# Optimization experiments

Hardware: AMD Instinct MI355X
Metric: run time of the kernel (lower is better)

Reference implementation:

```python
import jax, jax.numpy as jnp
import numpy as np

B, C, H, W = 32, 3, 224, 224
P = 14            # n_patches per side
PS = H // P       # 16
D = 768           # embed_size
NH = 12           # heads
DH = D // NH      # 64
L = 12            # n_blocks
FF = 4 * D
OUT = 1000
S = P * P + 1     # 197 tokens


def positional_encoding(seq_len, d):
    i = jnp.arange(seq_len, dtype=jnp.float32)[:, None]
    j = jnp.arange(d, dtype=jnp.float32)[None, :]
    je = jnp.where(j % 2 == 0, j, j - 1)
    ang = i / jnp.power(10000.0, je / d)
    return jnp.where(j % 2 == 0, jnp.sin(ang), jnp.cos(ang))


def layernorm(x, g, b, eps=1e-5):
    mu = jnp.mean(x, axis=-1, keepdims=True)
    var = jnp.var(x, axis=-1, keepdims=True)
    return (x - mu) * jax.lax.rsqrt(var + eps) * g + b


def setup_inputs() -> dict:
    key = jax.random.key(0)
    ks = jax.random.split(key, 20)
    s = 0.02
    inp = {
        'images': jax.random.normal(ks[0], (B, C, H, W), jnp.float32),
        'W_patch': jax.random.normal(ks[1], (D, C * PS * PS), jnp.float32) * s,
        'b_patch': jnp.zeros((D,), jnp.float32),
        'class_token': jax.random.uniform(ks[2], (1, D), jnp.float32),
        'ln1_g': jnp.ones((L, D), jnp.float32),
        'ln1_b': jnp.zeros((L, D), jnp.float32),
        'Wq': jax.random.normal(ks[3], (L, NH, DH, DH), jnp.float32) * s,
        'bq': jnp.zeros((L, NH, DH), jnp.float32),
        'Wk': jax.random.normal(ks[4], (L, NH, DH, DH), jnp.float32) * s,
        'bk': jnp.zeros((L, NH, DH), jnp.float32),
        'Wv': jax.random.normal(ks[5], (L, NH, DH, DH), jnp.float32) * s,
        'bv': jnp.zeros((L, NH, DH), jnp.float32),
        'ln2_g': jnp.ones((L, D), jnp.float32),
        'ln2_b': jnp.zeros((L, D), jnp.float32),
        'W1': jax.random.normal(ks[6], (L, FF, D), jnp.float32) * s,
        'b1': jnp.zeros((L, FF), jnp.float32),
        'W2': jax.random.normal(ks[7], (L, D, FF), jnp.float32) * s,
        'b2': jnp.zeros((L, D), jnp.float32),
        'Wo': jax.random.normal(ks[8], (OUT, D), jnp.float32) * s,
        'bo': jnp.zeros((OUT,), jnp.float32),
    }
    return inp


def reference(images, W_patch, b_patch, class_token, ln1_g, ln1_b,
              Wq, bq, Wk, bk, Wv, bv, ln2_g, ln2_b, W1, b1, W2, b2, Wo, bo):
    b = images.shape[0]
    # patch extraction: [B,C,P,ps,P,ps] -> [B,P*P, C*ps*ps] (flatten order C,h,w)
    patches = images.reshape(b, C, P, PS, P, PS).transpose(0, 2, 4, 1, 3, 5)
    patches = patches.reshape(b, P * P, C * PS * PS)
    tokens = patches @ W_patch.T + b_patch                     # [B, P^2, D]
    cls = jnp.broadcast_to(class_token[None], (b, 1, D))
    x = jnp.concatenate([cls, tokens], axis=1)                 # [B, S, D]
    x = x + positional_encoding(S, D)

    scale = 1.0 / jnp.sqrt(jnp.float32(DH))
    for l in range(L):
        h = layernorm(x, ln1_g[l], ln1_b[l])
        hh = h.reshape(b, S, NH, DH)
        q = jnp.einsum('bshd,hed->bshe', hh, Wq[l]) + bq[l]
        k = jnp.einsum('bshd,hed->bshe', hh, Wk[l]) + bk[l]
        v = jnp.einsum('bshd,hed->bshe', hh, Wv[l]) + bv[l]
        scores = jnp.einsum('bshe,bthe->bhst', q, k) * scale   # [B,H,S,S]
        attn = jax.nn.softmax(scores, axis=-1)
        o = jnp.einsum('bhst,bthe->bshe', attn, v).reshape(b, S, D)
        x = x + o
        h2 = layernorm(x, ln2_g[l], ln2_b[l])
        ff = jax.nn.gelu(h2 @ W1[l].T + b1[l], approximate=False) @ W2[l].T + b2[l]
        x = x + ff

    logits = x[:, 0] @ Wo.T + bo                               # [B, OUT]
    return jax.nn.softmax(logits, axis=-1)
```

## Files before the change

### kernel.cpp

```cpp
#include <hip/hip_runtime.h>
#include <math.h>

static constexpr int kB   = 32;
static constexpr int kC   = 3;
static constexpr int kH   = 224;
static constexpr int kW   = 224;
static constexpr int kP   = 14;
static constexpr int kPS  = 16;
static constexpr int kD   = 768;
static constexpr int kNH  = 12;
static constexpr int kDH  = 64;
static constexpr int kL   = 12;
static constexpr int kFF  = 3072;
static constexpr int kOUT = 1000;
static constexpr int kS   = 197;
static constexpr int kTOK = kB * kS;
static constexpr int kNP  = kP * kP;
static constexpr int kMP  = 6400;
static constexpr int kQKV = 3 * kD;

typedef unsigned short u16;
typedef __attribute__((ext_vector_type(4))) float f32x4;
typedef __attribute__((ext_vector_type(8))) short bf16x8;

__device__ __forceinline__ u16 f2bf(float x) {
    unsigned u = __float_as_uint(x);
    return (u16)((u + 0x7FFFu + ((u >> 16) & 1u)) >> 16);
}
__device__ __forceinline__ float bf2f(u16 x) {
    return __uint_as_float((unsigned)x << 16);
}
__device__ __forceinline__ void cp16_async(void* lds, const void* g) {
    __builtin_amdgcn_global_load_lds((const __attribute__((address_space(1))) unsigned*)g,
                                     (__attribute__((address_space(3))) unsigned*)lds,
                                     16, 0, 0);
}
__device__ __forceinline__ float gelu_f(float v) {
    float z = v * 0.70710678118654752f;
    float s = fabsf(z);
    float t = 1.0f / (1.0f + 0.3275911f * s);
    float p = t * (0.254829592f + t * (-0.284496736f +
              t * (1.421413741f + t * (-1.453152027f + t * 1.061405429f))));
    float e = p * __expf(-s * s);
    float erfv = (z < 0.0f) ? (e - 1.0f) : (1.0f - e);
    return 0.5f * v * (1.0f + erfv);
}

__global__ void vit_posenc(float* __restrict__ pos) {
    int idx = blockIdx.x * 256 + threadIdx.x;
    if (idx >= kS * kD) return;
    int s = idx / kD, d = idx % kD;
    int je = d & ~1;
    double p = pow(10000.0, (double)je / (double)kD);
    float ang = (float)((double)s / p);
    pos[idx] = (d & 1) ? cosf(ang) : sinf(ang);
}

__global__ void vit_im2col_bf16(const float* __restrict__ img, u16* __restrict__ patches) {
    long idx = (long)blockIdx.x * 256 + threadIdx.x;
    if (idx >= (long)kMP * kD) return;
    int col = (int)(idx % kD);
    long rp = idx / kD;
    if (rp >= (long)kB * kNP) { patches[idx] = 0; return; }
    int p = (int)(rp % kNP), b = (int)(rp / kNP);
    int c = col >> 8;
    int rem = col & 255;
    int i = rem >> 4, j = rem & 15;
    int py = p / kP, px = p % kP;
    patches[idx] = f2bf(img[(((long)b * kC + c) * kH + py * kPS + i) * kW + px * kPS + j]);
}

__global__ void vit_assemble(const float* __restrict__ tokens, const float* __restrict__ cls,
                             const float* __restrict__ pos, float* __restrict__ x) {
    long idx = (long)blockIdx.x * 256 + threadIdx.x;
    if (idx >= (long)kMP * kD) return;
    int d = (int)(idx % kD);
    long bs = idx / kD;
    if (bs >= kTOK) { x[idx] = 0.0f; return; }
    int s = (int)(bs % kS);
    long b = bs / kS;
    float v = (s == 0) ? cls[d] : tokens[((long)b * kNP + (s - 1)) * kD + d];
    x[idx] = v + pos[s * kD + d];
}

__global__ void cast_bf16(const float* __restrict__ in, u16* __restrict__ out, long n4) {
    long i = (long)blockIdx.x * 256 + threadIdx.x;
    if (i >= n4) return;
    float4 v = *(const float4*)(in + i * 4);
    *(ushort4*)(out + i * 4) = make_ushort4(f2bf(v.x), f2bf(v.y), f2bf(v.z), f2bf(v.w));
}
__global__ void cast2_bf16(const float* __restrict__ in1, const float* __restrict__ in2,
                           u16* __restrict__ out1, u16* __restrict__ out2, long n4each) {
    long i = (long)blockIdx.x * 256 + threadIdx.x;
    if (i >= 2 * n4each) return;
    const float* in = (i < n4each) ? in1 : in2;
    u16* out        = (i < n4each) ? out1 : out2;
    long j          = (i < n4each) ? i : i - n4each;
    float4 v = *(const float4*)(in + j * 4);
    *(ushort4*)(out + j * 4) = make_ushort4(f2bf(v.x), f2bf(v.y), f2bf(v.z), f2bf(v.w));
}

__global__ void zero_u16(u16* __restrict__ p, long n) {
    long i = (long)blockIdx.x * 256 + threadIdx.x;
    if (i < n) p[i] = 0;
}

__global__ void build_whb_all(const float* __restrict__ Wq, const float* __restrict__ Wk,
                              const float* __restrict__ Wv, const float* __restrict__ bq,
                              const float* __restrict__ bk, const float* __restrict__ bv,
                              u16* __restrict__ Wh, float* __restrict__ bh) {
    int idx = blockIdx.x * 256 + threadIdx.x;
    if (idx >= kL * kNH * 192 * 64) return;
    int d  = idx & 63;
    int r  = (idx >> 6) % 192;
    int lh = (idx >> 6) / 192;
    int sec = r >> 6, e = r & 63;
    const float* W = (sec == 0) ? Wq : (sec == 1) ? Wk : Wv;
    Wh[idx] = f2bf(W[((long)lh * 64 + e) * 64 + d]);
    if (d == 0) {
        const float* bs = (sec == 0) ? bq : (sec == 1) ? bk : bv;
        bh[lh * 192 + r] = bs[lh * 64 + e];
    }
}

__global__ __launch_bounds__(256) void vit_ln(const float* __restrict__ x,
                                              const float* __restrict__ g,
                                              const float* __restrict__ b,
                                              u16* __restrict__ out) {
    long t = blockIdx.x;
    const float* xr = x + t * kD;
    int tid = threadIdx.x;
    float v0 = xr[tid], v1 = xr[tid + 256], v2 = xr[tid + 512];
    float s  = v0 + v1 + v2;
    float sq = v0 * v0 + v1 * v1 + v2 * v2;
    #pragma unroll
    for (int o = 32; o; o >>= 1) { s += __shfl_xor(s, o); sq += __shfl_xor(sq, o); }
    __shared__ float red[8];
    int wid = tid >> 6, lane = tid & 63;
    if (lane == 0) { red[wid] = s; red[4 + wid] = sq; }
    __syncthreads();
    s  = red[0] + red[1] + red[2] + red[3];
    sq = red[4] + red[5] + red[6] + red[7];
    float mu  = s * (1.0f / kD);
    float var = sq * (1.0f / kD) - mu * mu;
    float rs  = rsqrtf(var + 1e-5f);
    u16* orow = out + t * kD;
    orow[tid]       = f2bf((v0 - mu) * rs * g[tid]       + b[tid]);
    orow[tid + 256] = f2bf((v1 - mu) * rs * g[tid + 256] + b[tid + 256]);
    orow[tid + 512] = f2bf((v2 - mu) * rs * g[tid + 512] + b[tid + 512]);
}

template <int EPI>
__global__ __launch_bounds__(256) void mm_bt(const u16* __restrict__ A, int lda,
                                             const u16* __restrict__ B, int ldb,
                                             const float* __restrict__ bias,
                                             const float* X, void* Cout, int ldc, int K) {
    __shared__ __align__(16) u16 As[3][4096];
    __shared__ __align__(16) u16 Bs[3][4096];

    const int gx = gridDim.x, gy = gridDim.y;
    const int nwg = gx * gy;
    const int disp = blockIdx.y * gx + blockIdx.x;
    const int q8 = nwg >> 3, r8 = nwg & 7;
    const int xcd = disp & 7, lot = disp >> 3;
    const int work = (xcd < r8 ? xcd * (q8 + 1) : r8 * (q8 + 1) + (xcd - r8) * q8) + lot;
    const int row0 = (work / gy) << 7;
    const int col0 = (work % gy) << 7;

    const int tid  = threadIdx.x;
    const int lane = tid & 63;
    const int wm = ((tid >> 6) >> 1) << 6;
    const int wn = ((tid >> 6) & 1) << 6;
    const int lr = lane & 15, lhi = lane >> 4;

    const int srow = tid >> 2;
    const int sch  = (((tid & 3) ^ ((srow >> 1) & 3)) << 3);
    const u16* Ag = A + (long)(row0 + srow) * lda + sch;
    const u16* Bg = B + (long)(col0 + srow) * ldb + sch;
    const long Astep = 64L * lda, Bstep = 64L * ldb;
    const int ldst = tid << 3;

    auto stage = [&](int buf, int k0) {
        cp16_async(&As[buf][ldst],        Ag + k0);
        cp16_async(&As[buf][ldst + 2048], Ag + Astep + k0);
        cp16_async(&Bs[buf][ldst],        Bg + k0);
        cp16_async(&Bs[buf][ldst + 2048], Bg + Bstep + k0);
    };
    stage(0, 0);
    stage(1, 32);

    f32x4 acc[4][4] = {};
    const int nk = K >> 5;
    const int rch = (lhi ^ ((lr >> 1) & 3)) << 3;
    int cur = 0;
    for (int t = 0; t < nk; t++) {
        if (t + 1 < nk) asm volatile("s_waitcnt vmcnt(4)" ::: "memory");
        else            asm volatile("s_waitcnt vmcnt(0)" ::: "memory");
        __builtin_amdgcn_sched_barrier(0);
        __builtin_amdgcn_s_barrier();
        bf16x8 af[4], bfr[4];
        #pragma unroll
        for (int m = 0; m < 4; m++)
            af[m] = *(const bf16x8*)&As[cur][(wm + (m << 4) + lr) * 32 + rch];
        #pragma unroll
        for (int n = 0; n < 4; n++)
            bfr[n] = *(const bf16x8*)&Bs[cur][(wn + (n << 4) + lr) * 32 + rch];
        if (t + 2 < nk) {
            int nb = cur + 2; if (nb >= 3) nb -= 3;
            stage(nb, (t + 2) << 5);
        }
        #pragma unroll
        for (int m = 0; m < 4; m++)
            #pragma unroll
            for (int n = 0; n < 4; n++)
                acc[m][n] = __builtin_amdgcn_mfma_f32_16x16x32_bf16(af[m], bfr[n], acc[m][n], 0, 0, 0);
        __builtin_amdgcn_s_barrier();
        cur = (cur + 1 == 3) ? 0 : cur + 1;
    }

    const int r0 = wm + (lhi << 2);
    const int cb = wn + lr;
    #pragma unroll
    for (int n = 0; n < 4; n++) {
        const int cc = col0 + cb + (n << 4);
        const float bv = bias[cc];
        #pragma unroll
        for (int m = 0; m < 4; m++) {
            #pragma unroll
            for (int r = 0; r < 4; r++) {
                const long idx = (long)(row0 + r0 + (m << 4) + r) * ldc + cc;
                float v = acc[m][n][r] + bv;
                if (EPI == 1) {
                    ((u16*)Cout)[idx] = f2bf(gelu_f(v));
                } else if (EPI == 2) {
                    ((float*)Cout)[idx] = v + X[idx];
                } else if (EPI == 3) {
                    ((u16*)Cout)[idx] = f2bf(v);
                } else {
                    ((float*)Cout)[idx] = v;
                }
            }
        }
    }
}

__global__ __launch_bounds__(256) void mm_qkv(const u16* __restrict__ hbm,
                                              const u16* __restrict__ Wh,
                                              const float* __restrict__ bh,
                                              u16* __restrict__ qkv) {
    const int h = blockIdx.y;
    const int row0 = blockIdx.x << 6;
    const int tid = threadIdx.x, lane = tid & 63, wave = tid >> 6;
    const int l15 = lane & 15, lhi = lane >> 4;
    const u16* Ab = hbm + h * kDH + (lhi << 3);
    const u16* Bb = Wh + (long)h * 192 * 64 + (lhi << 3);

    bf16x8 af[4][2];
    #pragma unroll
    for (int m = 0; m < 4; m++) {
        const u16* ap = Ab + (long)(row0 + (m << 4) + l15) * kD;
        af[m][0] = *(const bf16x8*)ap;
        af[m][1] = *(const bf16x8*)(ap + 32);
    }
    bf16x8 bfr[3][2];
    #pragma unroll
    for (int n = 0; n < 3; n++) {
        const u16* bp = Bb + (long)(wave * 48 + (n << 4) + l15) * 64;
        bfr[n][0] = *(const bf16x8*)bp;
        bfr[n][1] = *(const bf16x8*)(bp + 32);
    }
    f32x4 acc[4][3] = {};
    __builtin_amdgcn_s_setprio(1);
    #pragma unroll
    for (int m = 0; m < 4; m++)
        #pragma unroll
        for (int n = 0; n < 3; n++) {
            acc[m][n] = __builtin_amdgcn_mfma_f32_16x16x32_bf16(af[m][0], bfr[n][0], acc[m][n], 0, 0, 0);
            acc[m][n] = __builtin_amdgcn_mfma_f32_16x16x32_bf16(af[m][1], bfr[n][1], acc[m][n], 0, 0, 0);
        }
    __builtin_amdgcn_s_setprio(0);
    #pragma unroll
    for (int n = 0; n < 3; n++) {
        const int c = wave * 48 + (n << 4) + l15;
        const int sec = c >> 6, e = c & 63;
        const float bv = bh[h * 192 + c];
        const long gcol = (long)sec * kD + h * kDH + e;
        #pragma unroll
        for (int m = 0; m < 4; m++)
            #pragma unroll
            for (int i = 0; i < 4; i++) {
                const int r = row0 + (m << 4) + (lhi << 2) + i;
                qkv[(long)r * kQKV + gcol] = f2bf(acc[m][n][i] + bv);
            }
    }
}

__global__ __launch_bounds__(256) void vit_attn_fused(const u16* __restrict__ qkv,
                                                      float* __restrict__ x) {
    constexpr int SP = 224;
    constexpr int NT = 13;
    constexpr int LDP = 232;
    __shared__ u16 Plds[64][LDP];
    __shared__ u16 Vt[64][LDP];

    const int z = blockIdx.y, qt = blockIdx.x;
    const int b = z / kNH, h = z % kNH;
    const u16* base = qkv + (long)b * kS * kQKV;
    const u16* Qg = base + h * kDH;
    const u16* Kg = base + kD + h * kDH;
    const u16* Vg = base + 2 * kD + h * kDH;
    const int tid = threadIdx.x, lane = tid & 63, wave = tid >> 6;
    const int l15 = lane & 15, lhi = lane >> 4;

    for (int i = tid; i < (SP * kDH) / 4; i += 256) {
        int s  = i >> 4;
        int d0 = (i & 15) << 2;
        ushort4 v = *(const ushort4*)(Vg + (long)s * kQKV + d0);
        Vt[d0 + 0][s] = v.x; Vt[d0 + 1][s] = v.y;
        Vt[d0 + 2][s] = v.z; Vt[d0 + 3][s] = v.w;
    }

    const int qrow = (qt << 6) + (wave << 4) + l15;
    const u16* qrp = Qg + (long)qrow * kQKV + (lhi << 3);
    const bf16x8 qf0 = *(const bf16x8*)(qrp);
    const bf16x8 qf1 = *(const bf16x8*)(qrp + 32);

    f32x4 sc[NT];
    const u16* krp = Kg + (long)l15 * kQKV + (lhi << 3);
    __builtin_amdgcn_s_setprio(1);
    #pragma unroll
    for (int t = 0; t < NT; t++) {
        const u16* kp = krp + (long)(t << 4) * kQKV;
        bf16x8 kb0 = *(const bf16x8*)(kp);
        bf16x8 kb1 = *(const bf16x8*)(kp + 32);
        f32x4 a = {0.0f, 0.0f, 0.0f, 0.0f};
        a = __builtin_amdgcn_mfma_f32_16x16x32_bf16(qf0, kb0, a, 0, 0, 0);
        a = __builtin_amdgcn_mfma_f32_16x16x32_bf16(qf1, kb1, a, 0, 0, 0);
        sc[t] = a;
    }
    __builtin_amdgcn_s_setprio(0);

    float mx[4] = {-1e30f, -1e30f, -1e30f, -1e30f};
    #pragma unroll
    for (int t = 0; t < NT; t++) {
        const int c = (t << 4) + l15;
        #pragma unroll
        for (int q = 0; q < 4; q++) {
            float v = (c < kS) ? sc[t][q] * 0.125f : -1e30f;
            sc[t][q] = v;
            mx[q] = fmaxf(mx[q], v);
        }
    }
    #pragma unroll
    for (int o = 1; o < 16; o <<= 1)
        #pragma unroll
        for (int q = 0; q < 4; q++) mx[q] = fmaxf(mx[q], __shfl_xor(mx[q], o));
    float sum[4] = {0.0f, 0.0f, 0.0f, 0.0f};
    #pragma unroll
    for (int t = 0; t < NT; t++)
        #pragma unroll
        for (int q = 0; q < 4; q++) {
            float e = __expf(sc[t][q] - mx[q]);
            sc[t][q] = e;
            sum[q] += e;
        }
    #pragma unroll
    for (int o = 1; o < 16; o <<= 1)
        #pragma unroll
        for (int q = 0; q < 4; q++) sum[q] += __shfl_xor(sum[q], o);

    const int prow = (wave << 4) + (lhi << 2);
    #pragma unroll
    for (int t = 0; t < NT; t++)
        #pragma unroll
        for (int q = 0; q < 4; q++)
            Plds[prow + q][(t << 4) + l15] = f2bf(sc[t][q]);
    #pragma unroll
    for (int q = 0; q < 4; q++)
        Plds[prow + q][208 + l15] = 0;
    __syncthreads();

    f32x4 oacc[4] = {};
    const int arow = (wave << 4) + l15;
    const int koff = lhi << 3;
    __builtin_amdgcn_s_setprio(1);
    #pragma unroll
    for (int ks = 0; ks < 7; ks++) {
        bf16x8 pa = *(const bf16x8*)&Plds[arow][ks * 32 + koff];
        #pragma unroll
        for (int n = 0; n < 4; n++) {
            bf16x8 vb = *(const bf16x8*)&Vt[(n << 4) + l15][ks * 32 + koff];
            oacc[n] = __builtin_amdgcn_mfma_f32_16x16x32_bf16(pa, vb, oacc[n], 0, 0, 0);
        }
    }
    __builtin_amdgcn_s_setprio(0);

    const int orow0 = (qt << 6) + (wave << 4) + (lhi << 2);
    #pragma unroll
    for (int q = 0; q < 4; q++) {
        const int r = orow0 + q;
        if (r >= kS) continue;
        const float rinv = 1.0f / sum[q];
        float* xp = x + ((long)b * kS + r) * kD + h * kDH + l15;
        #pragma unroll
        for (int n = 0; n < 4; n++)
            xp[n << 4] += oacc[n][q] * rinv;
    }
}

template <int ACT, int RES>
__global__ __launch_bounds__(256) void vit_gemm(const float* __restrict__ A, long lda, long sAz,
                                                const float* __restrict__ B, long ldb, long sBz,
                                                const float* __restrict__ bias, long sbz,
                                                const float* __restrict__ R,
                                                float* __restrict__ C, long ldc, long sCz,
                                                int M, int N, int K) {
    __shared__ __align__(16) float As[16][64];
    __shared__ __align__(16) float Bs[16][64];
    long z = blockIdx.z;
    A += z * sAz;  B += z * sBz;  C += z * sCz;
    if (bias) bias += z * sbz;
    const float* Rp = nullptr;
    if (RES) Rp = R + z * sCz;

    int row0 = blockIdx.x * 64, col0 = blockIdx.y * 64;
    int tid = threadIdx.x;
    int lr = tid >> 2, lk = (tid & 3) << 2;
    int tm = tid >> 4, tn = tid & 15;
    float acc[4][4] = {};

    for (int k0 = 0; k0 < K; k0 += 16) {
        float4 a = {0, 0, 0, 0}, bb = {0, 0, 0, 0};
        int gr = row0 + lr;
        if (gr < M) a = *(const float4*)(A + (long)gr * lda + k0 + lk);
        int gc = col0 + lr;
        if (gc < N) bb = *(const float4*)(B + (long)gc * ldb + k0 + lk);
        __syncthreads();
        As[lk + 0][lr] = a.x;  As[lk + 1][lr] = a.y;  As[lk + 2][lr] = a.z;  As[lk + 3][lr] = a.w;
        Bs[lk + 0][lr] = bb.x; Bs[lk + 1][lr] = bb.y; Bs[lk + 2][lr] = bb.z; Bs[lk + 3][lr] = bb.w;
        __syncthreads();
        #pragma unroll
        for (int k = 0; k < 16; k++) {
            const float4 av = *reinterpret_cast<const float4*>(&As[k][tm << 2]);
            const float4 bv = *reinterpret_cast<const float4*>(&Bs[k][tn << 2]);
            float aa[4] = {av.x, av.y, av.z, av.w};
            float bw[4] = {bv.x, bv.y, bv.z, bv.w};
            #pragma unroll
            for (int i = 0; i < 4; i++)
                #pragma unroll
                for (int j = 0; j < 4; j++)
                    acc[i][j] = fmaf(aa[i], bw[j], acc[i][j]);
        }
    }
    #pragma unroll
    for (int i = 0; i < 4; i++) {
        int r = row0 + (tm << 2) + i;
        if (r >= M) continue;
        #pragma unroll
        for (int j = 0; j < 4; j++) {
            int c = col0 + (tn << 2) + j;
            if (c >= N) continue;
            float v = acc[i][j];
            if (bias) v += bias[c];
            if (ACT == 1) v = gelu_f(v);
            if (RES) v += Rp[(long)r * ldc + c];
            C[(long)r * ldc + c] = v;
        }
    }
}

__global__ __launch_bounds__(256) void vit_smout(const float* __restrict__ logits,
                                                 float* __restrict__ out) {
    int b = blockIdx.x;
    const float* p = logits + (long)b * kOUT;
    int tid = threadIdx.x;
    float v[4];
    float mx = -1e30f;
    #pragma unroll
    for (int i = 0; i < 4; i++) {
        int c = tid + (i << 8);
        v[i] = (c < kOUT) ? p[c] : -1e30f;
        mx = fmaxf(mx, v[i]);
    }
    #pragma unroll
    for (int o = 32; o; o >>= 1) mx = fmaxf(mx, __shfl_xor(mx, o));
    __shared__ float red[8];
    int wid = tid >> 6, lane = tid & 63;
    if (lane == 0) red[wid] = mx;
    __syncthreads();
    mx = fmaxf(fmaxf(red[0], red[1]), fmaxf(red[2], red[3]));
    float sum = 0.0f;
    #pragma unroll
    for (int i = 0; i < 4; i++) {
        int c = tid + (i << 8);
        if (c < kOUT) { v[i] = expf(v[i] - mx); sum += v[i]; }
    }
    #pragma unroll
    for (int o = 32; o; o >>= 1) sum += __shfl_xor(sum, o);
    __syncthreads();
    if (lane == 0) red[4 + wid] = sum;
    __syncthreads();
    sum = red[4] + red[5] + red[6] + red[7];
    float inv = 1.0f / sum;
    #pragma unroll
    for (int i = 0; i < 4; i++) {
        int c = tid + (i << 8);
        if (c < kOUT) out[(long)b * kOUT + c] = v[i] * inv;
    }
}

extern "C" void kernel_launch(void* const* d_in, const int* in_sizes, int n_in,
                              void* d_out, int out_size, void* d_ws, size_t ws_size,
                              hipStream_t stream) {
    (void)in_sizes; (void)n_in; (void)out_size;
    const float* images  = (const float*)d_in[0];
    const float* W_patch = (const float*)d_in[1];
    const float* b_patch = (const float*)d_in[2];
    const float* cls     = (const float*)d_in[3];
    const float* ln1_g   = (const float*)d_in[4];
    const float* ln1_b   = (const float*)d_in[5];
    const float* Wq      = (const float*)d_in[6];
    const float* bq      = (const float*)d_in[7];
    const float* Wk      = (const float*)d_in[8];
    const float* bk      = (const float*)d_in[9];
    const float* Wv      = (const float*)d_in[10];
    const float* bv      = (const float*)d_in[11];
    const float* ln2_g   = (const float*)d_in[12];
    const float* ln2_b   = (const float*)d_in[13];
    const float* W1      = (const float*)d_in[14];
    const float* b1      = (const float*)d_in[15];
    const float* W2      = (const float*)d_in[16];
    const float* b2      = (const float*)d_in[17];
    const float* Wo      = (const float*)d_in[18];
    const float* bo      = (const float*)d_in[19];

    char* wsB = (char*)d_ws;
    auto alloc = [&](size_t bytes) { char* p = wsB; wsB += (bytes + 255) & ~(size_t)255; return p; };
    float* pos    = (float*)alloc((size_t)kS * kD * 4);
    float* x      = (float*)alloc((size_t)kMP * kD * 4);
    u16*   hb     = (u16*)  alloc((size_t)kMP * kD * 2);
    u16*   qkvb   = (u16*)  alloc((size_t)kMP * kQKV * 2);
    u16*   ff1b   = (u16*)  alloc((size_t)kMP * kFF * 2);
    u16*   Whb    = (u16*)  alloc((size_t)kL * kNH * 192 * 64 * 2);
    u16*   Wpb    = (u16*)  alloc((size_t)kD * kD * 2);
    float* bhb    = (float*)alloc((size_t)kL * kNH * 192 * 4);
    float* logits = (float*)alloc((size_t)kB * kOUT * 4);

    const size_t perW  = (size_t)kFF * kD;
    const size_t used  = (size_t)(wsB - (char*)d_ws);
    const bool   hoist = ws_size >= used + 2 * kL * perW * 2 + (1u << 20);
    u16* W12b = (u16*)alloc(hoist ? 2 * kL * perW * 2 : 2 * perW * 2);

    float* tokens   = (float*)qkvb;
    u16*   patchesb = ff1b;

    vit_posenc<<<(kS * kD + 255) / 256, 256, 0, stream>>>(pos);
    vit_im2col_bf16<<<(int)(((long)kMP * kD) / 256), 256, 0, stream>>>(images, patchesb);
    cast_bf16<<<(kD * kD / 4 + 255) / 256, 256, 0, stream>>>(W_patch, Wpb, (long)kD * kD / 4);
    build_whb_all<<<(kL * kNH * 192 * 64 + 255) / 256, 256, 0, stream>>>(
        Wq, Wk, Wv, bq, bk, bv, Whb, bhb);
    zero_u16<<<(96 * kD + 255) / 256, 256, 0, stream>>>(hb + (long)kTOK * kD, 96L * kD);
    if (hoist)
        cast2_bf16<<<(int)((2 * kL * perW / 4 + 255) / 256), 256, 0, stream>>>(
            W1, W2, W12b, W12b + kL * perW, (long)kL * perW / 4);
    mm_bt<0><<<dim3(kMP / 128, kD / 128), 256, 0, stream>>>(
        patchesb, kD, Wpb, kD, b_patch, nullptr, tokens, kD, kD);
    vit_assemble<<<(int)(((long)kMP * kD) / 256), 256, 0, stream>>>(tokens, cls, pos, x);

    for (int l = 0; l < kL; l++) {
        u16* W1l = hoist ? (W12b + (size_t)l * perW)            : W12b;
        u16* W2l = hoist ? (W12b + (size_t)(kL + l) * perW)     : W12b + perW;
        if (!hoist)
            cast2_bf16<<<(int)((2 * perW / 4 + 255) / 256), 256, 0, stream>>>(
                W1 + (size_t)l * perW, W2 + (size_t)l * perW, W1l, W2l, (long)perW / 4);

        vit_ln<<<kTOK, 256, 0, stream>>>(x, ln1_g + (long)l * kD, ln1_b + (long)l * kD, hb);
        mm_qkv<<<dim3(kMP / 64, kNH), 256, 0, stream>>>(
            hb, Whb + (long)l * kNH * 192 * 64, bhb + (long)l * kNH * 192, qkvb);

        vit_attn_fused<<<dim3(4, kB * kNH), 256, 0, stream>>>(qkvb, x);

        vit_ln<<<kTOK, 256, 0, stream>>>(x, ln2_g + (long)l * kD, ln2_b + (long)l * kD, hb);
        mm_bt<1><<<dim3(kMP / 128, kFF / 128), 256, 0, stream>>>(
            hb, kD, W1l, kD, b1 + (long)l * kFF, nullptr, ff1b, kFF, kD);
        mm_bt<2><<<dim3(kMP / 128, kD / 128), 256, 0, stream>>>(
            ff1b, kFF, W2l, kFF, b2 + (long)l * kD, x, x, kD, kFF);
    }

    vit_gemm<0, 0><<<dim3(1, 16, 1), 256, 0, stream>>>(
        x, (long)kS * kD, 0, Wo, kD, 0, bo, 0, nullptr,
        logits, kOUT, 0, kB, kOUT, kD);
    vit_smout<<<kB, 256, 0, stream>>>(logits, (float*)d_out);
}
```

Measured before the change: 2.533 ms.

## Add 128x256 tile GEMM with XCD-aware scheduling for FF1

Adds mm_bt2, a 512-thread GEMM with a 128x256 output tile and three-stage async LDS staging. It remaps workgroups so consecutive tiles land on the same XCD, and the FF1 projection now uses it. The larger tile is meant to improve operand reuse and L2 locality, at the cost of more LDS per block and fewer blocks per CU. It also makes the weight cast a grid-stride loop with a fixed 2048 blocks and computes positional encoding in float with __expf instead of double pow, which may shift precision slightly.

```diff
diff --git a/kernel.cpp b/kernel.cpp
--- a/kernel.cpp
+++ b/kernel.cpp
@@ -51,8 +51,7 @@
     if (idx >= kS * kD) return;
     int s = idx / kD, d = idx % kD;
     int je = d & ~1;
-    double p = pow(10000.0, (double)je / (double)kD);
-    float ang = (float)((double)s / p);
+    float ang = (float)s * __expf((float)je * (-9.210340371976184f / 768.0f));
     pos[idx] = (d & 1) ? cosf(ang) : sinf(ang);
 }
 
@@ -91,13 +90,14 @@
 }
 __global__ void cast2_bf16(const float* __restrict__ in1, const float* __restrict__ in2,
                            u16* __restrict__ out1, u16* __restrict__ out2, long n4each) {
-    long i = (long)blockIdx.x * 256 + threadIdx.x;
-    if (i >= 2 * n4each) return;
-    const float* in = (i < n4each) ? in1 : in2;
-    u16* out        = (i < n4each) ? out1 : out2;
-    long j          = (i < n4each) ? i : i - n4each;
-    float4 v = *(const float4*)(in + j * 4);
-    *(ushort4*)(out + j * 4) = make_ushort4(f2bf(v.x), f2bf(v.y), f2bf(v.z), f2bf(v.w));
+    const long stride = (long)gridDim.x * 256;
+    for (long i = (long)blockIdx.x * 256 + threadIdx.x; i < 2 * n4each; i += stride) {
+        const float* in = (i < n4each) ? in1 : in2;
+        u16* out        = (i < n4each) ? out1 : out2;
+        long j          = (i < n4each) ? i : i - n4each;
+        float4 v = *(const float4*)(in + j * 4);
+        *(ushort4*)(out + j * 4) = make_ushort4(f2bf(v.x), f2bf(v.y), f2bf(v.z), f2bf(v.w));
+    }
 }
 
 __global__ void zero_u16(u16* __restrict__ p, long n) {
@@ -195,6 +195,100 @@
     int cur = 0;
     for (int t = 0; t < nk; t++) {
         if (t + 1 < nk) asm volatile("s_waitcnt vmcnt(4)" ::: "memory");
+        else            asm volatile("s_waitcnt vmcnt(0)" ::: "memory");
+        __builtin_amdgcn_sched_barrier(0);
+        __builtin_amdgcn_s_barrier();
+        bf16x8 af[4], bfr[4];
+        #pragma unroll
+        for (int m = 0; m < 4; m++)
+            af[m] = *(const bf16x8*)&As[cur][(wm + (m << 4) + lr) * 32 + rch];
+        #pragma unroll
+        for (int n = 0; n < 4; n++)
+            bfr[n] = *(const bf16x8*)&Bs[cur][(wn + (n << 4) + lr) * 32 + rch];
+        if (t + 2 < nk) {
+            int nb = cur + 2; if (nb >= 3) nb -= 3;
+            stage(nb, (t + 2) << 5);
+        }
+        #pragma unroll
+        for (int m = 0; m < 4; m++)
+            #pragma unroll
+            for (int n = 0; n < 4; n++)
+                acc[m][n] = __builtin_amdgcn_mfma_f32_16x16x32_bf16(af[m], bfr[n], acc[m][n], 0, 0, 0);
+        __builtin_amdgcn_s_barrier();
+        cur = (cur + 1 == 3) ? 0 : cur + 1;
+    }
+
+    const int r0 = wm + (lhi << 2);
+    const int cb = wn + lr;
+    #pragma unroll
+    for (int n = 0; n < 4; n++) {
+        const int cc = col0 + cb + (n << 4);
+        const float bv = bias[cc];
+        #pragma unroll
+        for (int m = 0; m < 4; m++) {
+            #pragma unroll
+            for (int r = 0; r < 4; r++) {
+                const long idx = (long)(row0 + r0 + (m << 4) + r) * ldc + cc;
+                float v = acc[m][n][r] + bv;
+                if (EPI == 1) {
+                    ((u16*)Cout)[idx] = f2bf(gelu_f(v));
+                } else if (EPI == 2) {
+                    ((float*)Cout)[idx] = v + X[idx];
+                } else if (EPI == 3) {
+                    ((u16*)Cout)[idx] = f2bf(v);
+                } else {
+                    ((float*)Cout)[idx] = v;
+                }
+            }
+        }
+    }
+}
+
+template <int EPI>
+__global__ __launch_bounds__(512, 4) void mm_bt2(const u16* __restrict__ A, int lda,
+                                                 const u16* __restrict__ B, int ldb,
+                                                 const float* __restrict__ bias,
+                                                 const float* X, void* Cout, int ldc, int K) {
+    __shared__ __align__(16) u16 As[3][4096];
+    __shared__ __align__(16) u16 Bs[3][8192];
+
+    const int gx = gridDim.x, gy = gridDim.y;
+    const int nwg = gx * gy;
+    const int disp = blockIdx.y * gx + blockIdx.x;
+    const int q8 = nwg >> 3, r8 = nwg & 7;
+    const int xcd = disp & 7, lot = disp >> 3;
+    const int work = (xcd < r8 ? xcd * (q8 + 1) : r8 * (q8 + 1) + (xcd - r8) * q8) + lot;
+    const int row0 = (work / gy) << 7;
+    const int col0 = (work % gy) << 8;
+
+    const int tid  = threadIdx.x;
+    const int lane = tid & 63;
+    const int wid  = tid >> 6;
+    const int wm = (wid >> 2) << 6;
+    const int wn = (wid & 3) << 6;
+    const int lr = lane & 15, lhi = lane >> 4;
+
+    const int srow = tid >> 2;
+    const int sch  = (((tid & 3) ^ ((srow >> 1) & 3)) << 3);
+    const u16* Ag = A + (long)(row0 + srow) * lda + sch;
+    const u16* Bg = B + (long)(col0 + srow) * ldb + sch;
+    const long Bstep = 128L * ldb;
+    const int ldst = tid << 3;
+
+    auto stage = [&](int buf, int k0) {
+        cp16_async(&As[buf][ldst],        Ag + k0);
+        cp16_async(&Bs[buf][ldst],        Bg + k0);
+        cp16_async(&Bs[buf][ldst + 4096], Bg + Bstep + k0);
+    };
+    stage(0, 0);
+    stage(1, 32);
+
+    f32x4 acc[4][4] = {};
+    const int nk = K >> 5;
+    const int rch = (lhi ^ ((lr >> 1) & 3)) << 3;
+    int cur = 0;
+    for (int t = 0; t < nk; t++) {
+        if (t + 1 < nk) asm volatile("s_waitcnt vmcnt(3)" ::: "memory");
         else            asm volatile("s_waitcnt vmcnt(0)" ::: "memory");
         __builtin_amdgcn_sched_barrier(0);
         __builtin_amdgcn_s_barrier();
@@ -561,7 +655,7 @@
         Wq, Wk, Wv, bq, bk, bv, Whb, bhb);
     zero_u16<<<(96 * kD + 255) / 256, 256, 0, stream>>>(hb + (long)kTOK * kD, 96L * kD);
     if (hoist)
-        cast2_bf16<<<(int)((2 * kL * perW / 4 + 255) / 256), 256, 0, stream>>>(
+        cast2_bf16<<<2048, 256, 0, stream>>>(
             W1, W2, W12b, W12b + kL * perW, (long)kL * perW / 4);
     mm_bt<0><<<dim3(kMP / 128, kD / 128), 256, 0, stream>>>(
         patchesb, kD, Wpb, kD, b_patch, nullptr, tokens, kD, kD);
@@ -571,7 +665,7 @@
         u16* W1l = hoist ? (W12b + (size_t)l * perW)            : W12b;
         u16* W2l = hoist ? (W12b + (size_t)(kL + l) * perW)     : W12b + perW;
         if (!hoist)
-            cast2_bf16<<<(int)((2 * perW / 4 + 255) / 256), 256, 0, stream>>>(
+            cast2_bf16<<<2048, 256, 0, stream>>>(
                 W1 + (size_t)l * perW, W2 + (size_t)l * perW, W1l, W2l, (long)perW / 4);
 
         vit_ln<<<kTOK, 256, 0, stream>>>(x, ln1_g + (long)l * kD, ln1_b + (long)l * kD, hb);
@@ -581,7 +675,7 @@
         vit_attn_fused<<<dim3(4, kB * kNH), 256, 0, stream>>>(qkvb, x);
 
         vit_ln<<<kTOK, 256, 0, stream>>>(x, ln2_g + (long)l * kD, ln2_b + (long)l * kD, hb);
-        mm_bt<1><<<dim3(kMP / 128, kFF / 128), 256, 0, stream>>>(
+        mm_bt2<1><<<dim3(kMP / 128, kFF / 256), 512, 0, stream>>>(
             hb, kD, W1l, kD, b1 + (long)l * kFF, nullptr, ff1b, kFF, kD);
         mm_bt<2><<<dim3(kMP / 128, kD / 128), 256, 0, stream>>>(
             ff1b, kFF, W2l, kFF, b2 + (long)l * kD, x, x, kD, kFF);
```

Measured after the change: 2.643 ms. +4.3%, slower.
